# Kernel tuning notes

Measured on AMD Instinct MI355X. Metric: run time of the kernel, lower is better.

## Reference

```python
import jax, jax.numpy as jnp
import numpy as np

IN_CAPS = 32
IN_CH = 8
OUT_CAPS = 10
OUT_CH = 16
NUM_ROUTING = 3
WID = 6
HEI = 6
BATCH = 64


def setup_inputs() -> dict:
    key = jax.random.key(0)
    k1, k2 = jax.random.split(key)
    u = jax.random.normal(k1, (BATCH, IN_CAPS, IN_CH, WID, HEI), dtype=jnp.float32)
    W = jax.random.normal(k2, (IN_CAPS, IN_CH, WID, HEI, OUT_CAPS, OUT_CH), dtype=jnp.float32) * 0.05
    return {"u": u, "W": W}


def reference(u, W):
    # u: [B, ic, ich, w, h]; W: [ic, ich, w, h, oc, och]
    B = u.shape[0]
    # _mul_1: broadcast multiply then fold (ich*w*h) into one axis
    u_hat = (u[..., None, None] * W[None]).reshape(
        B, IN_CAPS, IN_CH * WID * HEI, OUT_CAPS, OUT_CH
    )  # [B, ic, D, oc, och]
    u_sum = u_hat.sum(axis=2)            # [B, ic, oc, och] (used every iteration in _mul_2)
    u_dot = u_hat.sum(axis=(0, 2, 4))    # [ic, oc] (constant part of _dot)
    b_ij = jnp.zeros((IN_CAPS, OUT_CAPS), dtype=u.dtype)
    v_j = None
    for _ in range(NUM_ROUTING):
        c_ij = jax.nn.softmax(b_ij, axis=0)                     # softmax over in_capsules
        s_j = jnp.einsum('io,bioc->boc', c_ij, u_sum)           # [B, oc, och]
        # squash with GLOBAL L1 norm (torch .norm(1) over all elements) -- faithful to source
        n = jnp.abs(s_j).sum()
        v_j = (n * n) / (1.0 + n * n) * (s_j / n)               # [B, oc, och]
        agree = u_dot * v_j.sum(axis=(0, 2))[None, :]           # [ic, oc]
        b_ij = b_ij + jax.lax.stop_gradient(agree)              # torch uses .data (detached)
    return v_j
```

## Files before the change

### kernel.cpp

```cpp
#include <hip/hip_runtime.h>
#include <math.h>

#define B_   64
#define IC   32
#define D_   288
#define OC   10
#define OCH  16
#define J_   160
#define BJ   10240

__global__ __launch_bounds__(320) void k_usum(const float* __restrict__ u,
                                              const float* __restrict__ Wt,
                                              float* __restrict__ US,
                                              float* __restrict__ UDp,
                                              float* __restrict__ nacc,
                                              int* __restrict__ bar) {
    const int ic  = blockIdx.x & 31;
    const int bt  = blockIdx.x >> 5;
    const int tid = threadIdx.x;
    __shared__ float u_lds[4 * D_];
    __shared__ float part[640];
    __shared__ float ud_part[OC];
    if (tid < OC) ud_part[tid] = 0.f;
    if (blockIdx.x == 0 && tid == 0) {
        nacc[0] = 0.f; nacc[1] = 0.f; nacc[2] = 0.f;
        *bar = 0;
    }
    for (int idx = tid; idx < 288; idx += 320) {
        int b_sub = idx / 72;
        int f4    = idx - b_sub * 72;
        int b     = bt * 4 + b_sub;
        ((float4*)u_lds)[idx] =
            ((const float4*)(u + (size_t)(b * IC + ic) * D_))[f4];
    }
    __syncthreads();
    const int j4    = tid % 40;
    const int b_sub = (tid / 40) & 3;
    const int dh    = tid / 160;
    const float4* wp = (const float4*)(Wt + (size_t)ic * D_ * J_)
                       + (size_t)dh * 144 * 40 + j4;
    const float*  ur = u_lds + b_sub * D_ + dh * 144;
    float ax = 0.f, ay = 0.f, az = 0.f, aw = 0.f;
    for (int d0 = 0; d0 < 144; d0 += 8) {
        float4 w0 = wp[(d0 + 0) * 40];
        float4 w1 = wp[(d0 + 1) * 40];
        float4 w2 = wp[(d0 + 2) * 40];
        float4 w3 = wp[(d0 + 3) * 40];
        float4 w4 = wp[(d0 + 4) * 40];
        float4 w5 = wp[(d0 + 5) * 40];
        float4 w6 = wp[(d0 + 6) * 40];
        float4 w7 = wp[(d0 + 7) * 40];
        float u0 = ur[d0 + 0], u1 = ur[d0 + 1], u2 = ur[d0 + 2], u3 = ur[d0 + 3];
        float u4 = ur[d0 + 4], u5 = ur[d0 + 5], u6 = ur[d0 + 6], u7 = ur[d0 + 7];
        ax += u0 * w0.x; ay += u0 * w0.y; az += u0 * w0.z; aw += u0 * w0.w;
        ax += u1 * w1.x; ay += u1 * w1.y; az += u1 * w1.z; aw += u1 * w1.w;
        ax += u2 * w2.x; ay += u2 * w2.y; az += u2 * w2.z; aw += u2 * w2.w;
        ax += u3 * w3.x; ay += u3 * w3.y; az += u3 * w3.z; aw += u3 * w3.w;
        ax += u4 * w4.x; ay += u4 * w4.y; az += u4 * w4.z; aw += u4 * w4.w;
        ax += u5 * w5.x; ay += u5 * w5.y; az += u5 * w5.z; aw += u5 * w5.w;
        ax += u6 * w6.x; ay += u6 * w6.y; az += u6 * w6.z; aw += u6 * w6.w;
        ax += u7 * w7.x; ay += u7 * w7.y; az += u7 * w7.z; aw += u7 * w7.w;
    }
    if (dh == 1) ((float4*)part)[tid - 160] = make_float4(ax, ay, az, aw);
    __syncthreads();
    if (dh == 0) {
        float4 p = ((float4*)part)[tid];
        ax += p.x; ay += p.y; az += p.z; aw += p.w;
        ((float4*)(US + (size_t)ic * BJ + (bt * 4 + b_sub) * J_))[j4] =
            make_float4(ax, ay, az, aw);
        float g = ax + ay + az + aw;
        g += __shfl_xor(g, 1);
        g += __shfl_xor(g, 2);
        if ((tid & 3) == 0) atomicAdd(&ud_part[j4 >> 2], g);
    }
    __syncthreads();
    if (tid < OC) UDp[blockIdx.x * OC + tid] = ud_part[tid];
}

__global__ __launch_bounds__(1024) void k_route(const float* __restrict__ US,
                                                const float* __restrict__ UDp,
                                                float* __restrict__ nacc,
                                                int* __restrict__ bar,
                                                float* __restrict__ out) {
    const int tid = threadIdx.x;
    const int i   = tid & 31;
    const int o   = tid >> 5;
    __shared__ float cij[OC * IC];
    __shared__ float wred[16];
    __shared__ float nsh;
    float udv = 0.f;
    if (tid < 320) {
        #pragma unroll
        for (int bt = 0; bt < 16; ++bt) udv += UDp[(bt * 32 + i) * OC + o];
    }
    const int t  = blockIdx.x * 1024 + tid;
    const int ot = (t >> 4) % OC;
    float bij = 0.f;
    for (int q = 0; q < 3; ++q) {
        float cs = 0.f;
        if (tid < 320) {
            float m = bij;
            m = fmaxf(m, __shfl_xor(m, 16, 32));
            m = fmaxf(m, __shfl_xor(m,  8, 32));
            m = fmaxf(m, __shfl_xor(m,  4, 32));
            m = fmaxf(m, __shfl_xor(m,  2, 32));
            m = fmaxf(m, __shfl_xor(m,  1, 32));
            float e  = __expf(bij - m);
            float se = e;
            se += __shfl_xor(se, 16, 32);
            se += __shfl_xor(se,  8, 32);
            se += __shfl_xor(se,  4, 32);
            se += __shfl_xor(se,  2, 32);
            se += __shfl_xor(se,  1, 32);
            float c = e / se;
            cij[o * IC + i] = c;
            cs = c * udv;
            cs += __shfl_xor(cs, 16, 32);
            cs += __shfl_xor(cs,  8, 32);
            cs += __shfl_xor(cs,  4, 32);
            cs += __shfl_xor(cs,  2, 32);
            cs += __shfl_xor(cs,  1, 32);
        }
        __syncthreads();
        float s = 0.f;
        {
            const float* usp = US + t;
            const float* cp  = cij + ot * IC;
            #pragma unroll
            for (int ii = 0; ii < IC; ++ii) s += cp[ii] * usp[(size_t)ii * BJ];
        }
        float a = fabsf(s);
        #pragma unroll
        for (int off = 32; off; off >>= 1) a += __shfl_down(a, off);
        if ((tid & 63) == 0) wred[tid >> 6] = a;
        __syncthreads();
        if (tid == 0) {
            float blk = 0.f;
            #pragma unroll
            for (int w = 0; w < 16; ++w) blk += wred[w];
            atomicAdd(nacc + q, blk);
            __threadfence();
            atomicAdd(bar, 1);
            while (__hip_atomic_load(bar, __ATOMIC_ACQUIRE,
                                     __HIP_MEMORY_SCOPE_AGENT) < 10 * (q + 1))
                __builtin_amdgcn_s_sleep(1);
            nsh = __hip_atomic_load(nacc + q, __ATOMIC_RELAXED,
                                    __HIP_MEMORY_SCOPE_AGENT);
        }
        __syncthreads();
        const float n  = nsh;
        const float n2 = n * n;
        if (q < 2) {
            if (tid < 320) bij += udv * ((n2 / (1.f + n2)) * (cs / n));
        } else {
            out[t] = (n2 / (1.f + n2)) * (s / n);
        }
    }
}

extern "C" void kernel_launch(void* const* d_in, const int* in_sizes, int n_in,
                              void* d_out, int out_size, void* d_ws, size_t ws_size,
                              hipStream_t stream) {
    (void)in_sizes; (void)n_in; (void)out_size; (void)ws_size;
    const float* u  = (const float*)d_in[0];
    const float* Wt = (const float*)d_in[1];
    float* ws   = (float*)d_ws;
    float* US   = ws;
    float* UDp  = ws + 327680;
    float* nacc = ws + 332800;
    int*   bar  = (int*)(ws + 332803);

    k_usum<<<dim3(512), dim3(320), 0, stream>>>(u, Wt, US, UDp, nacc, bar);
    k_route<<<dim3(10), dim3(1024), 0, stream>>>(US, UDp, nacc, bar, (float*)d_out);
}
```

Before: 81.01 us.

## Replace spin-barrier routing kernel with per-iteration kernel launches

Splits the single 10-block routing kernel, which used a global atomic spin barrier between routing iterations, into separate iteration kernels plus an output kernel, using kernel boundaries for grid-wide sync. Iteration 0 is specialised so uniform softmax coefficients become a plain mean, and each iteration kernel runs on 32 blocks of 320 threads instead of 10 blocks of 1024. This trades spin-wait and atomic-polling cost for extra launch overheads and an intermediate S2 buffer write and read.

```diff
diff --git a/kernel.cpp b/kernel.cpp
--- a/kernel.cpp
+++ b/kernel.cpp
@@ -9,12 +9,12 @@
 #define J_   160
 #define BJ   10240
 
+
 __global__ __launch_bounds__(320) void k_usum(const float* __restrict__ u,
                                               const float* __restrict__ Wt,
                                               float* __restrict__ US,
                                               float* __restrict__ UDp,
-                                              float* __restrict__ nacc,
-                                              int* __restrict__ bar) {
+                                              float* __restrict__ nacc) {
     const int ic  = blockIdx.x & 31;
     const int bt  = blockIdx.x >> 5;
     const int tid = threadIdx.x;
@@ -24,7 +24,6 @@
     if (tid < OC) ud_part[tid] = 0.f;
     if (blockIdx.x == 0 && tid == 0) {
         nacc[0] = 0.f; nacc[1] = 0.f; nacc[2] = 0.f;
-        *bar = 0;
     }
     for (int idx = tid; idx < 288; idx += 320) {
         int b_sub = idx / 72;
@@ -77,85 +76,157 @@
     if (tid < OC) UDp[blockIdx.x * OC + tid] = ud_part[tid];
 }
 
-__global__ __launch_bounds__(1024) void k_route(const float* __restrict__ US,
-                                                const float* __restrict__ UDp,
-                                                float* __restrict__ nacc,
-                                                int* __restrict__ bar,
-                                                float* __restrict__ out) {
+__global__ __launch_bounds__(320) void k_iter0(const float* __restrict__ US,
+                                               const float* __restrict__ UDp,
+                                               float* __restrict__ nacc,
+                                               float* __restrict__ UD,
+                                               float* __restrict__ css) {
+    const int tid = threadIdx.x;
+    const int t   = blockIdx.x * 320 + tid;
+    __shared__ float wred[5];
+    float s = 0.f;
+    {
+        const float* usp = US + t;
+        #pragma unroll
+        for (int ii = 0; ii < IC; ++ii) s += usp[(size_t)ii * BJ];
+        s *= 0.03125f;
+    }
+    float a = fabsf(s);
+    #pragma unroll
+    for (int off = 32; off; off >>= 1) a += __shfl_down(a, off);
+    if ((tid & 63) == 0) wred[tid >> 6] = a;
+    if (blockIdx.x == 0) {
+        const int i = tid & 31;
+        const int o = tid >> 5;
+        float udv = 0.f;
+        #pragma unroll
+        for (int bt = 0; bt < 16; ++bt) udv += UDp[(bt * 32 + i) * OC + o];
+        UD[tid] = udv;
+        float cs = udv;
+        cs += __shfl_xor(cs, 16, 32);
+        cs += __shfl_xor(cs,  8, 32);
+        cs += __shfl_xor(cs,  4, 32);
+        cs += __shfl_xor(cs,  2, 32);
+        cs += __shfl_xor(cs,  1, 32);
+        if (i == 0) css[o] = cs * 0.03125f;
+    }
+    __syncthreads();
+    if (tid == 0)
+        atomicAdd(nacc + 0, wred[0] + wred[1] + wred[2] + wred[3] + wred[4]);
+}
+
+__global__ __launch_bounds__(320) void k_iter1(const float* __restrict__ US,
+                                               const float* __restrict__ UD,
+                                               float* __restrict__ css,
+                                               float* __restrict__ nacc) {
     const int tid = threadIdx.x;
     const int i   = tid & 31;
     const int o   = tid >> 5;
+    const int t   = blockIdx.x * 320 + tid;
     __shared__ float cij[OC * IC];
-    __shared__ float wred[16];
-    __shared__ float nsh;
-    float udv = 0.f;
-    if (tid < 320) {
-        #pragma unroll
-        for (int bt = 0; bt < 16; ++bt) udv += UDp[(bt * 32 + i) * OC + o];
-    }
-    const int t  = blockIdx.x * 1024 + tid;
-    const int ot = (t >> 4) % OC;
-    float bij = 0.f;
-    for (int q = 0; q < 3; ++q) {
-        float cs = 0.f;
-        if (tid < 320) {
-            float m = bij;
-            m = fmaxf(m, __shfl_xor(m, 16, 32));
-            m = fmaxf(m, __shfl_xor(m,  8, 32));
-            m = fmaxf(m, __shfl_xor(m,  4, 32));
-            m = fmaxf(m, __shfl_xor(m,  2, 32));
-            m = fmaxf(m, __shfl_xor(m,  1, 32));
-            float e  = __expf(bij - m);
-            float se = e;
-            se += __shfl_xor(se, 16, 32);
-            se += __shfl_xor(se,  8, 32);
-            se += __shfl_xor(se,  4, 32);
-            se += __shfl_xor(se,  2, 32);
-            se += __shfl_xor(se,  1, 32);
-            float c = e / se;
-            cij[o * IC + i] = c;
-            cs = c * udv;
-            cs += __shfl_xor(cs, 16, 32);
-            cs += __shfl_xor(cs,  8, 32);
-            cs += __shfl_xor(cs,  4, 32);
-            cs += __shfl_xor(cs,  2, 32);
-            cs += __shfl_xor(cs,  1, 32);
-        }
-        __syncthreads();
-        float s = 0.f;
-        {
-            const float* usp = US + t;
-            const float* cp  = cij + ot * IC;
-            #pragma unroll
-            for (int ii = 0; ii < IC; ++ii) s += cp[ii] * usp[(size_t)ii * BJ];
-        }
-        float a = fabsf(s);
-        #pragma unroll
-        for (int off = 32; off; off >>= 1) a += __shfl_down(a, off);
-        if ((tid & 63) == 0) wred[tid >> 6] = a;
-        __syncthreads();
-        if (tid == 0) {
-            float blk = 0.f;
-            #pragma unroll
-            for (int w = 0; w < 16; ++w) blk += wred[w];
-            atomicAdd(nacc + q, blk);
-            __threadfence();
-            atomicAdd(bar, 1);
-            while (__hip_atomic_load(bar, __ATOMIC_ACQUIRE,
-                                     __HIP_MEMORY_SCOPE_AGENT) < 10 * (q + 1))
-                __builtin_amdgcn_s_sleep(1);
-            nsh = __hip_atomic_load(nacc + q, __ATOMIC_RELAXED,
-                                    __HIP_MEMORY_SCOPE_AGENT);
-        }
-        __syncthreads();
-        const float n  = nsh;
-        const float n2 = n * n;
-        if (q < 2) {
-            if (tid < 320) bij += udv * ((n2 / (1.f + n2)) * (cs / n));
-        } else {
-            out[t] = (n2 / (1.f + n2)) * (s / n);
-        }
-    }
+    __shared__ float wred[5];
+    const float udv = UD[tid];
+    const float n0  = nacc[0];
+    const float n02 = n0 * n0;
+    float bij = udv * ((n02 / (1.f + n02)) * (css[o] / n0));
+    float m = bij;
+    m = fmaxf(m, __shfl_xor(m, 16, 32));
+    m = fmaxf(m, __shfl_xor(m,  8, 32));
+    m = fmaxf(m, __shfl_xor(m,  4, 32));
+    m = fmaxf(m, __shfl_xor(m,  2, 32));
+    m = fmaxf(m, __shfl_xor(m,  1, 32));
+    float e  = __expf(bij - m);
+    float se = e;
+    se += __shfl_xor(se, 16, 32);
+    se += __shfl_xor(se,  8, 32);
+    se += __shfl_xor(se,  4, 32);
+    se += __shfl_xor(se,  2, 32);
+    se += __shfl_xor(se,  1, 32);
+    float c = e / se;
+    cij[o * IC + i] = c;
+    float cs = c * udv;
+    cs += __shfl_xor(cs, 16, 32);
+    cs += __shfl_xor(cs,  8, 32);
+    cs += __shfl_xor(cs,  4, 32);
+    cs += __shfl_xor(cs,  2, 32);
+    cs += __shfl_xor(cs,  1, 32);
+    if (blockIdx.x == 0 && i == 0) css[10 + o] = cs;
+    __syncthreads();
+    float s = 0.f;
+    {
+        const int ot = (t >> 4) % OC;
+        const float* usp = US + t;
+        const float* cp  = cij + ot * IC;
+        #pragma unroll
+        for (int ii = 0; ii < IC; ++ii) s += cp[ii] * usp[(size_t)ii * BJ];
+    }
+    float a = fabsf(s);
+    #pragma unroll
+    for (int off = 32; off; off >>= 1) a += __shfl_down(a, off);
+    if ((tid & 63) == 0) wred[tid >> 6] = a;
+    __syncthreads();
+    if (tid == 0)
+        atomicAdd(nacc + 1, wred[0] + wred[1] + wred[2] + wred[3] + wred[4]);
+}
+
+__global__ __launch_bounds__(320) void k_iter2(const float* __restrict__ US,
+                                               const float* __restrict__ UD,
+                                               const float* __restrict__ css,
+                                               float* __restrict__ nacc,
+                                               float* __restrict__ S2) {
+    const int tid = threadIdx.x;
+    const int i   = tid & 31;
+    const int o   = tid >> 5;
+    const int t   = blockIdx.x * 320 + tid;
+    __shared__ float cij[OC * IC];
+    __shared__ float wred[5];
+    const float udv = UD[tid];
+    const float n0  = nacc[0];
+    const float n1  = nacc[1];
+    const float n02 = n0 * n0;
+    const float n12 = n1 * n1;
+    float bij = udv * ((n02 / (1.f + n02)) * (css[o] / n0));
+    bij      += udv * ((n12 / (1.f + n12)) * (css[10 + o] / n1));
+    float m = bij;
+    m = fmaxf(m, __shfl_xor(m, 16, 32));
+    m = fmaxf(m, __shfl_xor(m,  8, 32));
+    m = fmaxf(m, __shfl_xor(m,  4, 32));
+    m = fmaxf(m, __shfl_xor(m,  2, 32));
+    m = fmaxf(m, __shfl_xor(m,  1, 32));
+    float e  = __expf(bij - m);
+    float se = e;
+    se += __shfl_xor(se, 16, 32);
+    se += __shfl_xor(se,  8, 32);
+    se += __shfl_xor(se,  4, 32);
+    se += __shfl_xor(se,  2, 32);
+    se += __shfl_xor(se,  1, 32);
+    cij[o * IC + i] = e / se;
+    __syncthreads();
+    float s = 0.f;
+    {
+        const int ot = (t >> 4) % OC;
+        const float* usp = US + t;
+        const float* cp  = cij + ot * IC;
+        #pragma unroll
+        for (int ii = 0; ii < IC; ++ii) s += cp[ii] * usp[(size_t)ii * BJ];
+    }
+    S2[t] = s;
+    float a = fabsf(s);
+    #pragma unroll
+    for (int off = 32; off; off >>= 1) a += __shfl_down(a, off);
+    if ((tid & 63) == 0) wred[tid >> 6] = a;
+    __syncthreads();
+    if (tid == 0)
+        atomicAdd(nacc + 2, wred[0] + wred[1] + wred[2] + wred[3] + wred[4]);
+}
+
+__global__ __launch_bounds__(1024) void k_out(const float* __restrict__ S2,
+                                              const float* __restrict__ nacc,
+                                              float* __restrict__ out) {
+    const int t = blockIdx.x * 1024 + threadIdx.x;
+    const float n  = nacc[2];
+    const float n2 = n * n;
+    out[t] = (n2 / (1.f + n2)) * (S2[t] / n);
 }
 
 extern "C" void kernel_launch(void* const* d_in, const int* in_sizes, int n_in,
@@ -168,8 +239,13 @@
     float* US   = ws;
     float* UDp  = ws + 327680;
     float* nacc = ws + 332800;
-    int*   bar  = (int*)(ws + 332803);
-
-    k_usum<<<dim3(512), dim3(320), 0, stream>>>(u, Wt, US, UDp, nacc, bar);
-    k_route<<<dim3(10), dim3(1024), 0, stream>>>(US, UDp, nacc, bar, (float*)d_out);
-}
+    float* UD   = ws + 332816;
+    float* css  = ws + 333136;
+    float* S2   = ws + 333184;
+
+    k_usum <<<dim3(512), dim3(320),  0, stream>>>(u, Wt, US, UDp, nacc);
+    k_iter0<<<dim3(32),  dim3(320),  0, stream>>>(US, UDp, nacc, UD, css);
+    k_iter1<<<dim3(32),  dim3(320),  0, stream>>>(US, UD, css, nacc);
+    k_iter2<<<dim3(32),  dim3(320),  0, stream>>>(US, UD, css, nacc, S2);
+    k_out  <<<dim3(10),  dim3(1024), 0, stream>>>(S2, nacc, (float*)d_out);
+}
```

After: 82.99 us. 2.4% more time.
